# Optimization experiments

Measured on AMD Instinct MI355X. Metric: run time of the kernel, lower is better.

Reference implementation:

```python
import jax, jax.numpy as jnp
from jax import lax
import numpy as np

LATENT = 16
HIDDEN = 16  # latent_dim > 8 -> 16
NUM_ATTRACTORS = 64
GRAVITY = 0.01
INPUT_DIM = 300
B, S = 32, 2048
N_ITERS = 20


def setup_inputs() -> dict:
    key = jax.random.key(0)
    ks = jax.random.split(key, 12)
    sc = lambda fan_in: 1.0 / np.sqrt(fan_in)
    return {
        "inputs": jax.random.normal(ks[0], (B, S, INPUT_DIM), dtype=jnp.float32),
        "enc_w1": jax.random.normal(ks[1], (INPUT_DIM, HIDDEN), dtype=jnp.float32) * sc(INPUT_DIM),
        "enc_b1": jnp.zeros((HIDDEN,), dtype=jnp.float32),
        "enc_w2": jax.random.normal(ks[2], (HIDDEN, LATENT), dtype=jnp.float32) * sc(HIDDEN),
        "enc_b2": jnp.zeros((LATENT,), dtype=jnp.float32),
        "attractors": jax.random.normal(ks[3], (NUM_ATTRACTORS, LATENT), dtype=jnp.float32) * 0.1,
        "dec_w1": jax.random.normal(ks[4], (LATENT, HIDDEN), dtype=jnp.float32) * sc(LATENT),
        "dec_b1": jnp.zeros((HIDDEN,), dtype=jnp.float32),
        "dec_w2": jax.random.normal(ks[5], (HIDDEN, INPUT_DIM), dtype=jnp.float32) * sc(HIDDEN),
        "dec_b2": jnp.zeros((INPUT_DIM,), dtype=jnp.float32),
        "mass_w": jax.random.normal(ks[6], (LATENT, 1), dtype=jnp.float32) * sc(LATENT),
        "mass_b": jnp.zeros((1,), dtype=jnp.float32),
    }


def reference(inputs, enc_w1, enc_b1, enc_w2, enc_b2, attractors,
              dec_w1, dec_b1, dec_w2, dec_b2, mass_w, mass_b):
    b, s, _ = inputs.shape
    # encoder: Linear(300,16) -> ReLU -> Linear(16,latent)
    h = jax.nn.relu(jnp.einsum('bsi,ih->bsh', inputs, enc_w1) + enc_b1)
    emb = jnp.einsum('bsh,hd->bsd', h, enc_w2) + enc_b2  # [B,S,D]

    def step(pos, _):
        # pos: [B,S,D]; attractors: [A,D]
        diff = attractors[None, None, :, :] - pos[:, :, None, :]          # [B,S,A,D]
        dist = jnp.sqrt(jnp.sum(diff * diff, axis=-1, keepdims=True)) + 1e-6
        forces = jnp.sum(GRAVITY * diff / (dist * dist), axis=2)          # [B,S,D]
        new_pos = pos + 0.1 * forces
        change = jnp.sqrt(jnp.sum((new_pos - pos) ** 2))
        return new_pos, change

    # torch code breaks if change < 1e-6; with random data this never fires,
    # so the fixed 20-iteration scan is equivalent.
    positions, changes = lax.scan(step, emb, None, length=N_ITERS)

    attractor_field = positions.mean(axis=1)                              # [B,D]
    rec = jax.nn.relu(attractor_field @ dec_w1 + dec_b1) @ dec_w2 + dec_b2  # [B,300]
    reconstructions = jnp.broadcast_to(rec[:, None, :], (b, s, INPUT_DIM))
    masses = jax.nn.sigmoid(attractor_field @ mass_w + mass_b)            # [B,1]
    final_change = changes[-1]
    return attractor_field, reconstructions, masses, final_change
```

## Files before the change

### kernel.cpp

```cpp
#include <hip/hip_runtime.h>
#include <cmath>

#define BB 32
#define SS 2048
#define IND 300
#define HID 16
#define LAT 16
#define NA 64
#define NITER 20
#define GRAV 0.01f

#define OFF_FIELD 0
#define OFF_REC   512
#define OFF_MASS  (512 + BB*SS*IND)
#define OFF_CHG   (OFF_MASS + BB)

#define WS_FIELD 0
#define WS_CHG   512

typedef __attribute__((ext_vector_type(8))) __bf16 bf16x8;
typedef __attribute__((ext_vector_type(4))) __bf16 bf16x4;
typedef __attribute__((ext_vector_type(2))) __bf16 bf16x2;
typedef __attribute__((ext_vector_type(4))) float f32x4;
typedef __attribute__((ext_vector_type(4))) unsigned uint4v;

#define HST 40

__device__ __forceinline__ unsigned pk_bf16(float lo, float hi) {
    bf16x2 t; t[0] = (__bf16)lo; t[1] = (__bf16)hi;
    return __builtin_bit_cast(unsigned, t);
}

__global__ __launch_bounds__(256, 4)
void k_fused(const float* __restrict__ x,  const float* __restrict__ w1,
             const float* __restrict__ b1, const float* __restrict__ w2,
             const float* __restrict__ b2, const float* __restrict__ att,
             float* __restrict__ ws)
{
    __shared__ __align__(16) __bf16 hl[4][16 * HST];
    __shared__ float red[4][LAT];
    __shared__ float redc[4];

    const int tid  = threadIdx.x;
    const int wave = tid >> 6, lane = tid & 63;
    const int quad = lane >> 4, col = lane & 15;
    const int tok  = blockIdx.x * 64 + wave * 16 + col;

    const float* xr = x + (size_t)tok * IND;
    f32x4 xv[10][2];
    #pragma unroll
    for (int s = 0; s < 5; ++s) {
        const float* xp = xr + s * 32 + quad * 8;
        xv[s][0] = *(const f32x4*)(xp);
        xv[s][1] = *(const f32x4*)(xp + 4);
    }
    __builtin_amdgcn_sched_barrier(0x7);
    #pragma unroll
    for (int s = 5; s < 9; ++s) {
        const float* xp = xr + s * 32 + quad * 8;
        xv[s][0] = *(const f32x4*)(xp);
        xv[s][1] = *(const f32x4*)(xp + 4);
    }
    {
        const f32x4 z = {0.f, 0.f, 0.f, 0.f};
        xv[9][0] = z; xv[9][1] = z;
        if (quad == 0) {
            xv[9][0] = *(const f32x4*)(xr + 288);
            xv[9][1] = *(const f32x4*)(xr + 292);
        } else if (quad == 1) {
            xv[9][0] = *(const f32x4*)(xr + 296);
        }
    }

    const f32x4 zf = {0.f, 0.f, 0.f, 0.f};
    bf16x8 ones8;
    #pragma unroll
    for (int e = 0; e < 8; ++e) ones8[e] = (__bf16)1.0f;

    bf16x8 aS[4];
    #pragma unroll
    for (int i = 0; i < 4; ++i) {
        const int arow = 32 * (i >> 1) + 8 * (col >> 2) + 4 * (i & 1) + (col & 3);
        f32x4 av = *(const f32x4*)(att + arow * LAT + quad * 4);
        #pragma unroll
        for (int m = 0; m < 4; ++m) {
            aS[i][2 * m]     = (__bf16)(-2.0f * av[m]);
            aS[i][2 * m + 1] = (__bf16)1.0f;
        }
    }
    f32x4 sanvP[4];
    {
        float nrm[4];
        #pragma unroll
        for (int i0 = 0; i0 < 4; ++i0) {
            const float* ar = att + (16 * i0 + col) * LAT;
            float s = 0.f;
            #pragma unroll
            for (int k = 0; k < LAT; ++k) s = fmaf(ar[k], ar[k], s);
            nrm[i0] = s;
        }
        float nrmSel[2];
        nrmSel[0] = (quad & 2) ? nrm[1] : nrm[0];
        nrmSel[1] = (quad & 2) ? nrm[3] : nrm[2];
        #pragma unroll
        for (int i = 0; i < 4; ++i)
            #pragma unroll
            for (int r = 0; r < 4; ++r) {
                const int src = (quad << 4) | (8 * (quad & 1) + 4 * (i & 1) + r);
                sanvP[i][r] = __shfl(nrmSel[i >> 1], src);
            }
    }
    bf16x8 aF[2];
    #pragma unroll
    for (int h = 0; h < 2; ++h)
        #pragma unroll
        for (int j = 0; j < 8; ++j)
            aF[h][j] = (__bf16)att[(32 * h + quad * 8 + j) * LAT + col];

    f32x4 p;
    {
        const float b1c = b1[col];
        f32x4 hacc = {b1c, b1c, b1c, b1c};
        #pragma unroll
        for (int s = 0; s < 10; ++s) {
            bf16x8 af, wf;
            #pragma unroll
            for (int e = 0; e < 4; ++e) {
                af[e]     = (__bf16)xv[s][0][e];
                af[4 + e] = (__bf16)xv[s][1][e];
            }
            if (s < 9) {
                #pragma unroll
                for (int j = 0; j < 8; ++j)
                    wf[j] = (__bf16)w1[(s * 32 + quad * 8 + j) * HID + col];
            } else {
                #pragma unroll
                for (int j = 0; j < 8; ++j)
                    wf[j] = (quad * 8 + j < 12)
                          ? (__bf16)w1[(288 + quad * 8 + j) * HID + col]
                          : (__bf16)0.f;
            }
            hacc = __builtin_amdgcn_mfma_f32_16x16x32_bf16(af, wf, hacc, 0, 0, 0);
        }

        __bf16* myh = hl[wave];
        #pragma unroll
        for (int r = 0; r < 4; ++r)
            myh[(quad * 4 + r) * HST + col] = (__bf16)fmaxf(hacc[r], 0.f);

        bf16x8 w2tf;
        #pragma unroll
        for (int j = 0; j < 8; ++j) {
            const int k = quad * 8 + j;
            w2tf[j] = (k < HID) ? (__bf16)w2[k * LAT + col] : (__bf16)0.f;
        }
        bf16x8 bh;
        #pragma unroll
        for (int e = 0; e < 8; ++e) bh[e] = (__bf16)0.f;
        if (quad < 2)
            bh = *(const bf16x8*)(myh + col * HST + quad * 8);
        f32x4 pacc = *(const f32x4*)(b2 + quad * 4);
        p = __builtin_amdgcn_mfma_f32_16x16x32_bf16(w2tf, bh, pacc, 0, 0, 0);
    }

    float cd = 0.f;
    #pragma unroll 1
    for (int it = 0; it < NITER; ++it) {
        bf16x8 bp;
        #pragma unroll
        for (int m = 0; m < 4; ++m) {
            float v = p[m];
            bp[2 * m]     = (__bf16)v;
            bp[2 * m + 1] = (__bf16)(v * v);
        }
        f32x4 sf[4];
        #pragma unroll
        for (int i = 0; i < 4; ++i)
            sf[i] = __builtin_amdgcn_mfma_f32_16x16x32_bf16(aS[i], bp, zf, 0, 0, 0);

        float w[4][4];
        #pragma unroll
        for (int i = 0; i < 4; ++i)
            #pragma unroll
            for (int r = 0; r < 4; ++r)
                w[i][r] = __builtin_amdgcn_rcpf(sf[i][r] + sanvP[i][r]);

        uint4v u0 = { pk_bf16(w[0][0], w[0][1]), pk_bf16(w[0][2], w[0][3]),
                      pk_bf16(w[1][0], w[1][1]), pk_bf16(w[1][2], w[1][3]) };
        uint4v u1 = { pk_bf16(w[2][0], w[2][1]), pk_bf16(w[2][2], w[2][3]),
                      pk_bf16(w[3][0], w[3][1]), pk_bf16(w[3][2], w[3][3]) };
        bf16x8 bw0 = __builtin_bit_cast(bf16x8, u0);
        bf16x8 bw1 = __builtin_bit_cast(bf16x8, u1);

        f32x4 F  = __builtin_amdgcn_mfma_f32_16x16x32_bf16(aF[0], bw0, zf, 0, 0, 0);
        F  = __builtin_amdgcn_mfma_f32_16x16x32_bf16(aF[1], bw1, F,  0, 0, 0);
        f32x4 F2 = __builtin_amdgcn_mfma_f32_16x16x32_bf16(ones8, bw0, zf, 0, 0, 0);
        F2 = __builtin_amdgcn_mfma_f32_16x16x32_bf16(ones8, bw1, F2, 0, 0, 0);

        const bool last = (it == NITER - 1);
        #pragma unroll
        for (int r = 0; r < 4; ++r) {
            float np = fmaf(p[r], fmaf(F2[r], -0.1f * GRAV, 1.0f),
                            (0.1f * GRAV) * F[r]);
            if (last) { float d = np - p[r]; cd = fmaf(d, d, cd); }
            p[r] = np;
        }
    }

    f32x4 fs = p;
    #pragma unroll
    for (int m = 1; m <= 8; m <<= 1)
        #pragma unroll
        for (int r = 0; r < 4; ++r) fs[r] += __shfl_xor(fs[r], m);
    if (col == 0) {
        #pragma unroll
        for (int r = 0; r < 4; ++r) red[wave][quad * 4 + r] = fs[r];
    }
    float c2 = cd;
    c2 += __shfl_xor(c2, 1);  c2 += __shfl_xor(c2, 2);  c2 += __shfl_xor(c2, 4);
    c2 += __shfl_xor(c2, 8);  c2 += __shfl_xor(c2, 16); c2 += __shfl_xor(c2, 32);
    if (lane == 0) redc[wave] = c2;
    __syncthreads();

    const int b = blockIdx.x >> 5;
    if (tid < LAT) {
        float v = red[0][tid] + red[1][tid] + red[2][tid] + red[3][tid];
        atomicAdd(ws + WS_FIELD + b * LAT + tid, v);
    }
    if (tid == 32)
        atomicAdd(ws + WS_CHG + (blockIdx.x & 63),
                  redc[0] + redc[1] + redc[2] + redc[3]);
}

#define CHUNK 8192
#define CPB   (SS * IND / CHUNK)
__global__ __launch_bounds__(256)
void k_bcast(const float* __restrict__ dw1, const float* __restrict__ db1,
             const float* __restrict__ dw2, const float* __restrict__ db2,
             const float* __restrict__ mw,  const float* __restrict__ mb,
             const float* __restrict__ ws, float* __restrict__ out)
{
    __shared__ float sf[LAT];
    __shared__ float sh[HID];
    __shared__ float schg[64];
    __shared__ __align__(16) float srow[IND];
    const int blk = blockIdx.x;
    const int b = blk / CPB, c = blk % CPB;
    const int t = threadIdx.x;

    if (t < LAT) {
        float f = ws[WS_FIELD + b * LAT + t] * (1.f / SS);
        sf[t] = f;
        if (c == 0) out[OFF_FIELD + b * LAT + t] = f;
    }
    if (blk == 0 && t < 64) schg[t] = ws[WS_CHG + t];
    __syncthreads();
    if (t < HID) {
        float a = db1[t];
        #pragma unroll
        for (int d = 0; d < LAT; ++d) a = fmaf(sf[d], dw1[d * HID + t], a);
        sh[t] = fmaxf(a, 0.f);
    }
    if (c == 0 && t == 32) {
        float a = mb[0];
        #pragma unroll
        for (int d = 0; d < LAT; ++d) a = fmaf(sf[d], mw[d], a);
        out[OFF_MASS + b] = 1.f / (1.f + expf(-a));
    }
    if (blk == 0 && t == 33) {
        float s = 0.f;
        #pragma unroll
        for (int i = 0; i < 64; ++i) s += schg[i];
        out[OFF_CHG] = sqrtf(s);
    }
    __syncthreads();
    if (t < IND) {
        float a = db2[t];
        #pragma unroll
        for (int j = 0; j < HID; ++j) a = fmaf(sh[j], dw2[j * IND + t], a);
        srow[t] = a;
    }
    if (t < IND - 256) {
        const int tc = t + 256;
        float a2 = db2[tc];
        #pragma unroll
        for (int j = 0; j < HID; ++j) a2 = fmaf(sh[j], dw2[j * IND + tc], a2);
        srow[tc] = a2;
    }
    __syncthreads();
    f32x4* o = (f32x4*)(out + OFF_REC + (size_t)b * (SS * IND) + (size_t)c * CHUNK);
    #pragma unroll
    for (int i = 0; i < CHUNK / 4 / 256; ++i) {
        const int o4 = i * 256 + t;
        const int r  = (c * CHUNK + o4 * 4) % IND;
        f32x4 v = *(const f32x4*)(srow + r);
        __builtin_nontemporal_store(v, o + o4);
    }
}

extern "C" void kernel_launch(void* const* d_in, const int* in_sizes, int n_in,
                              void* d_out, int out_size, void* d_ws, size_t ws_size,
                              hipStream_t stream)
{
    const float* x   = (const float*)d_in[0];
    const float* ew1 = (const float*)d_in[1];
    const float* eb1 = (const float*)d_in[2];
    const float* ew2 = (const float*)d_in[3];
    const float* eb2 = (const float*)d_in[4];
    const float* att = (const float*)d_in[5];
    const float* dw1 = (const float*)d_in[6];
    const float* db1 = (const float*)d_in[7];
    const float* dw2 = (const float*)d_in[8];
    const float* db2 = (const float*)d_in[9];
    const float* mw  = (const float*)d_in[10];
    const float* mb  = (const float*)d_in[11];
    float* out = (float*)d_out;
    float* ws  = (float*)d_ws;

    (void)hipMemsetAsync(ws, 0, (WS_CHG + 64) * sizeof(float), stream);
    k_fused<<<BB * SS / 64, 256, 0, stream>>>(x, ew1, eb1, ew2, eb2, att, ws);
    k_bcast<<<BB * CPB, 256, 0, stream>>>(dw1, db1, dw2, db2, mw, mb, ws, out);
}
```

Baseline: 191.8 us.

## Split fused encoder/gravity kernel and duplicate tokens across MFMA columns for occupancy

```diff
diff --git a/kernel.cpp b/kernel.cpp
--- a/kernel.cpp
+++ b/kernel.cpp
@@ -32,14 +32,11 @@
 }
 
 __global__ __launch_bounds__(256, 4)
-void k_fused(const float* __restrict__ x,  const float* __restrict__ w1,
-             const float* __restrict__ b1, const float* __restrict__ w2,
-             const float* __restrict__ b2, const float* __restrict__ att,
-             float* __restrict__ ws)
+void k_enc(const float* __restrict__ x,  const float* __restrict__ w1,
+           const float* __restrict__ b1, const float* __restrict__ w2,
+           const float* __restrict__ b2, float* __restrict__ pbuf)
 {
     __shared__ __align__(16) __bf16 hl[4][16 * HST];
-    __shared__ float red[4][LAT];
-    __shared__ float redc[4];
 
     const int tid  = threadIdx.x;
     const int wave = tid >> 6, lane = tid & 63;
@@ -49,14 +46,7 @@
     const float* xr = x + (size_t)tok * IND;
     f32x4 xv[10][2];
     #pragma unroll
-    for (int s = 0; s < 5; ++s) {
-        const float* xp = xr + s * 32 + quad * 8;
-        xv[s][0] = *(const f32x4*)(xp);
-        xv[s][1] = *(const f32x4*)(xp + 4);
-    }
-    __builtin_amdgcn_sched_barrier(0x7);
-    #pragma unroll
-    for (int s = 5; s < 9; ++s) {
+    for (int s = 0; s < 9; ++s) {
         const float* xp = xr + s * 32 + quad * 8;
         xv[s][0] = *(const f32x4*)(xp);
         xv[s][1] = *(const f32x4*)(xp + 4);
@@ -72,7 +62,66 @@
         }
     }
 
-    const f32x4 zf = {0.f, 0.f, 0.f, 0.f};
+    const float b1c = b1[col];
+    f32x4 hacc = {b1c, b1c, b1c, b1c};
+    #pragma unroll
+    for (int s = 0; s < 10; ++s) {
+        bf16x8 af, wf;
+        #pragma unroll
+        for (int e = 0; e < 4; ++e) {
+            af[e]     = (__bf16)xv[s][0][e];
+            af[4 + e] = (__bf16)xv[s][1][e];
+        }
+        if (s < 9) {
+            #pragma unroll
+            for (int j = 0; j < 8; ++j)
+                wf[j] = (__bf16)w1[(s * 32 + quad * 8 + j) * HID + col];
+        } else {
+            #pragma unroll
+            for (int j = 0; j < 8; ++j)
+                wf[j] = (quad * 8 + j < 12)
+                      ? (__bf16)w1[(288 + quad * 8 + j) * HID + col]
+                      : (__bf16)0.f;
+        }
+        hacc = __builtin_amdgcn_mfma_f32_16x16x32_bf16(af, wf, hacc, 0, 0, 0);
+    }
+
+    __bf16* myh = hl[wave];
+    #pragma unroll
+    for (int r = 0; r < 4; ++r)
+        myh[(quad * 4 + r) * HST + col] = (__bf16)fmaxf(hacc[r], 0.f);
+
+    bf16x8 w2tf;
+    #pragma unroll
+    for (int j = 0; j < 8; ++j) {
+        const int k = quad * 8 + j;
+        w2tf[j] = (k < HID) ? (__bf16)w2[k * LAT + col] : (__bf16)0.f;
+    }
+    bf16x8 bh;
+    #pragma unroll
+    for (int e = 0; e < 8; ++e) bh[e] = (__bf16)0.f;
+    if (quad < 2)
+        bh = *(const bf16x8*)(myh + col * HST + quad * 8);
+    f32x4 pacc = *(const f32x4*)(b2 + quad * 4);
+    f32x4 p = __builtin_amdgcn_mfma_f32_16x16x32_bf16(w2tf, bh, pacc, 0, 0, 0);
+
+    ((f32x4*)pbuf)[(size_t)tok * 4 + quad] = p;
+}
+
+__global__ __launch_bounds__(256, 8)
+void k_grav(const float* __restrict__ att, const float* __restrict__ pbuf,
+            float* __restrict__ ws)
+{
+    __shared__ float red[4][LAT];
+    __shared__ float redc[4];
+
+    const int tid  = threadIdx.x;
+    const int wave = tid >> 6, lane = tid & 63;
+    const int quad = lane >> 4, col = lane & 15;
+    const int tok  = blockIdx.x * 32 + wave * 8 + (col & 7);
+
+    f32x4 p = ((const f32x4*)pbuf)[(size_t)tok * 4 + quad];
+
     bf16x8 ones8;
     #pragma unroll
     for (int e = 0; e < 8; ++e) ones8[e] = (__bf16)1.0f;
@@ -117,52 +166,7 @@
         for (int j = 0; j < 8; ++j)
             aF[h][j] = (__bf16)att[(32 * h + quad * 8 + j) * LAT + col];
 
-    f32x4 p;
-    {
-        const float b1c = b1[col];
-        f32x4 hacc = {b1c, b1c, b1c, b1c};
-        #pragma unroll
-        for (int s = 0; s < 10; ++s) {
-            bf16x8 af, wf;
-            #pragma unroll
-            for (int e = 0; e < 4; ++e) {
-                af[e]     = (__bf16)xv[s][0][e];
-                af[4 + e] = (__bf16)xv[s][1][e];
-            }
-            if (s < 9) {
-                #pragma unroll
-                for (int j = 0; j < 8; ++j)
-                    wf[j] = (__bf16)w1[(s * 32 + quad * 8 + j) * HID + col];
-            } else {
-                #pragma unroll
-                for (int j = 0; j < 8; ++j)
-                    wf[j] = (quad * 8 + j < 12)
-                          ? (__bf16)w1[(288 + quad * 8 + j) * HID + col]
-                          : (__bf16)0.f;
-            }
-            hacc = __builtin_amdgcn_mfma_f32_16x16x32_bf16(af, wf, hacc, 0, 0, 0);
-        }
-
-        __bf16* myh = hl[wave];
-        #pragma unroll
-        for (int r = 0; r < 4; ++r)
-            myh[(quad * 4 + r) * HST + col] = (__bf16)fmaxf(hacc[r], 0.f);
-
-        bf16x8 w2tf;
-        #pragma unroll
-        for (int j = 0; j < 8; ++j) {
-            const int k = quad * 8 + j;
-            w2tf[j] = (k < HID) ? (__bf16)w2[k * LAT + col] : (__bf16)0.f;
-        }
-        bf16x8 bh;
-        #pragma unroll
-        for (int e = 0; e < 8; ++e) bh[e] = (__bf16)0.f;
-        if (quad < 2)
-            bh = *(const bf16x8*)(myh + col * HST + quad * 8);
-        f32x4 pacc = *(const f32x4*)(b2 + quad * 4);
-        p = __builtin_amdgcn_mfma_f32_16x16x32_bf16(w2tf, bh, pacc, 0, 0, 0);
-    }
-
+    const f32x4 zf = {0.f, 0.f, 0.f, 0.f};
     float cd = 0.f;
     #pragma unroll 1
     for (int it = 0; it < NITER; ++it) {
@@ -176,14 +180,14 @@
         f32x4 sf[4];
         #pragma unroll
         for (int i = 0; i < 4; ++i)
-            sf[i] = __builtin_amdgcn_mfma_f32_16x16x32_bf16(aS[i], bp, zf, 0, 0, 0);
+            sf[i] = __builtin_amdgcn_mfma_f32_16x16x32_bf16(aS[i], bp, sanvP[i], 0, 0, 0);
 
         float w[4][4];
         #pragma unroll
         for (int i = 0; i < 4; ++i)
             #pragma unroll
             for (int r = 0; r < 4; ++r)
-                w[i][r] = __builtin_amdgcn_rcpf(sf[i][r] + sanvP[i][r]);
+                w[i][r] = __builtin_amdgcn_rcpf(sf[i][r]);
 
         uint4v u0 = { pk_bf16(w[0][0], w[0][1]), pk_bf16(w[0][2], w[0][3]),
                       pk_bf16(w[1][0], w[1][1]), pk_bf16(w[1][2], w[1][3]) };
@@ -214,15 +218,15 @@
         for (int r = 0; r < 4; ++r) fs[r] += __shfl_xor(fs[r], m);
     if (col == 0) {
         #pragma unroll
-        for (int r = 0; r < 4; ++r) red[wave][quad * 4 + r] = fs[r];
+        for (int r = 0; r < 4; ++r) red[wave][quad * 4 + r] = 0.5f * fs[r];
     }
     float c2 = cd;
     c2 += __shfl_xor(c2, 1);  c2 += __shfl_xor(c2, 2);  c2 += __shfl_xor(c2, 4);
     c2 += __shfl_xor(c2, 8);  c2 += __shfl_xor(c2, 16); c2 += __shfl_xor(c2, 32);
-    if (lane == 0) redc[wave] = c2;
+    if (lane == 0) redc[wave] = 0.5f * c2;
     __syncthreads();
 
-    const int b = blockIdx.x >> 5;
+    const int b = blockIdx.x >> 6;
     if (tid < LAT) {
         float v = red[0][tid] + red[1][tid] + red[2][tid] + red[3][tid];
         atomicAdd(ws + WS_FIELD + b * LAT + tid, v);
@@ -316,8 +320,10 @@
     const float* mb  = (const float*)d_in[11];
     float* out = (float*)d_out;
     float* ws  = (float*)d_ws;
+    float* pbuf = out + OFF_REC;
 
     (void)hipMemsetAsync(ws, 0, (WS_CHG + 64) * sizeof(float), stream);
-    k_fused<<<BB * SS / 64, 256, 0, stream>>>(x, ew1, eb1, ew2, eb2, att, ws);
+    k_enc <<<BB * SS / 64,  256, 0, stream>>>(x, ew1, eb1, ew2, eb2, pbuf);
+    k_grav<<<BB * SS / 32,  256, 0, stream>>>(att, pbuf, ws);
     k_bcast<<<BB * CPB, 256, 0, stream>>>(dw1, db1, dw2, db2, mw, mb, ws, out);
 }
```

New measurement: 220.3 us. 1.15x slower.
